# Performance work log

Hardware: AMD Instinct MI355X
Metric: run time of the kernel (lower is better)

The kernel has to match this reference:

```python
import jax, jax.numpy as jnp
import numpy as np
from jax import lax

B, N, M, NCLS = 16, 8192, 64, 80          # batch, anchors, GT boxes, classes
M_W, M_H = 640, 640                       # config.model_in_sz
CLASS_ID = 0                              # config.objective_class_id
PROB_T = 0.0                              # prob_threshold default
IOU_MATCH = 0.5                           # GT<->pred matching threshold
NMS_THR = 0.5                             # NMS IoU threshold
EPS = 1e-7


def xywh2xyxy(x):
    cx, cy, w, h = x[..., 0], x[..., 1], x[..., 2], x[..., 3]
    return jnp.stack([cx - w / 2, cy - h / 2, cx + w / 2, cy + h / 2], axis=-1)


def box_iou(a, b):
    # torchvision-style IoU (no +1), a: (M,4), b: (N,4) -> (M,N)
    area_a = (a[:, 2] - a[:, 0]) * (a[:, 3] - a[:, 1])
    area_b = (b[:, 2] - b[:, 0]) * (b[:, 3] - b[:, 1])
    lt = jnp.maximum(a[:, None, :2], b[None, :, :2])
    rb = jnp.minimum(a[:, None, 2:], b[None, :, 2:])
    wh = jnp.clip(rb - lt, 0)
    inter = wh[..., 0] * wh[..., 1]
    return inter / (area_a[:, None] + area_b[None, :] - inter)


def setup_inputs() -> dict:
    key = jax.random.key(0)
    k1, k2, k3, k4, k5 = jax.random.split(key, 5)
    # GT labels: [class_id, cx, cy, w, h] normalized to [0,1]
    cxy = jax.random.uniform(k1, (B, M, 2), minval=0.2, maxval=0.8)
    wh = jax.random.uniform(k2, (B, M, 2), minval=0.05, maxval=0.25)
    cls = jnp.zeros((B, M, 1), jnp.float32)
    label_batch = jnp.concatenate([cls, cxy, wh], axis=-1)  # (B, M, 5)
    # Predictions: each anchor is a GT box (pixel xywh) + small noise, so
    # IoU>=0.5 matching and NMS actually fire.
    gt_idx = jnp.arange(N) % M
    scale = jnp.array([M_W, M_H, M_W, M_H], jnp.float32)
    base = label_batch[:, gt_idx, 1:] * scale               # (B, N, 4)
    pred_xywh = base + jax.random.normal(k3, (B, N, 4)) * 2.0
    obj = jax.random.uniform(k4, (B, N, 1), minval=0.1, maxval=1.0)
    cls_logits = jax.random.uniform(k5, (B, N, NCLS))
    output = jnp.concatenate([pred_xywh, obj, cls_logits], axis=-1)  # (B,N,85)
    return {"output": output, "label_batch": label_batch}


def nms_keep(boxes, scores, valid):
    # Greedy NMS over a padded candidate set. `valid` marks real candidates;
    # invalid entries get -inf score and can never suppress anything.
    n = boxes.shape[0]
    order = jnp.argsort(jnp.where(valid, scores, -jnp.inf))[::-1]
    b = boxes[order]
    v = valid[order]
    x1, y1, x2, y2 = b[:, 0], b[:, 1], b[:, 2], b[:, 3]
    area = (x2 - x1 + 1) * (y2 - y1 + 1)   # +1 convention, as in the source nms
    pos = jnp.arange(n)

    def body(i, supp):
        active = v[i] & jnp.logical_not(supp[i])
        xx1 = jnp.maximum(x1[i], x1)
        yy1 = jnp.maximum(y1[i], y1)
        xx2 = jnp.minimum(x2[i], x2)
        yy2 = jnp.minimum(y2[i], y2)
        inter = jnp.clip(xx2 - xx1 + 1, 0) * jnp.clip(yy2 - yy1 + 1, 0)
        iou = inter / (area[i] + area - inter + EPS)
        return supp | (active & (pos > i) & (iou > NMS_THR))

    supp = lax.fori_loop(0, n, body, jnp.zeros(n, dtype=bool))
    return v & jnp.logical_not(supp), order


def _per_image(out, lab):
    pred_boxes = xywh2xyxy(out[:, :4])                      # (N,4) pixel xyxy
    obj = out[:, 4]
    logits = out[:, 5 + CLASS_ID] * obj                     # class prob * objectness
    scale = jnp.array([M_W, M_H, M_W, M_H], out.dtype)
    gt = jnp.clip(xywh2xyxy(lab[:, 1:]), 0, 1) * scale      # (M,4) pixel xyxy
    iou = box_iou(gt, pred_boxes)                           # (M,N)
    # candidate = passes prob threshold AND overlaps some GT with IoU>=0.5
    valid = (obj >= PROB_T) & jnp.any(iou >= IOU_MATCH, axis=0)
    keep, order = nms_keep(lax.stop_gradient(pred_boxes),
                           lax.stop_gradient(logits), valid)
    kept = keep.astype(out.dtype)
    return jnp.sum(logits[order] * kept) / jnp.sum(kept)


def reference(output, label_batch):
    loss = jax.vmap(_per_image)(output, label_batch)        # (B,)
    return loss[None, :]                                    # (1, B)
```

## Files before the change

### kernel.cpp

```cpp
#include <hip/hip_runtime.h>
#include <math.h>

#define BB 16
#define NN 8192
#define MM 64
#define ROW 85
#define EPS_F 1e-7f

#define NT1 256
#define NT2 1024
#define NW  16
#define CPW 4
#define CAPB 8

typedef unsigned long long u64;

__global__ void prep_kernel(const float* __restrict__ outp,
                            const float* __restrict__ lab,
                            float4* __restrict__ boxes,
                            float* __restrict__ keys) {
    __shared__ float4 gbox[MM];
    __shared__ float garea[MM];
    const int b = blockIdx.x;
    const int tid = threadIdx.x;
    if (tid < MM) {
        const float* lr = lab + ((size_t)b * MM + tid) * 5;
        float cx = lr[1], cy = lr[2], w = lr[3], h = lr[4];
        float x1 = fminf(fmaxf(cx - w * 0.5f, 0.f), 1.f) * 640.f;
        float y1 = fminf(fmaxf(cy - h * 0.5f, 0.f), 1.f) * 640.f;
        float x2 = fminf(fmaxf(cx + w * 0.5f, 0.f), 1.f) * 640.f;
        float y2 = fminf(fmaxf(cy + h * 0.5f, 0.f), 1.f) * 640.f;
        gbox[tid] = make_float4(x1, y1, x2, y2);
        garea[tid] = (x2 - x1) * (y2 - y1);
    }
    __syncthreads();
    const int n = blockIdx.y * NT1 + tid;
    const float* row = outp + ((size_t)b * NN + n) * ROW;
    float cx = row[0], cy = row[1], w = row[2], h = row[3];
    float obj = row[4], c0 = row[5];
    float px1 = cx - w * 0.5f, py1 = cy - h * 0.5f;
    float px2 = cx + w * 0.5f, py2 = cy + h * 0.5f;
    float pa = (px2 - px1) * (py2 - py1);

    const int m0 = n & (MM - 1);
    bool match;
    {
        float4 g = gbox[m0];
        float iw = fmaxf(fminf(px2, g.z) - fmaxf(px1, g.x), 0.f);
        float ih = fmaxf(fminf(py2, g.w) - fmaxf(py1, g.y), 0.f);
        float inter = iw * ih;
        match = (inter / (garea[m0] + pa - inter) >= 0.5f);
    }
    if (!match) {
        for (int m = 0; m < MM; ++m) {
            float4 g = gbox[m];
            float iw = fmaxf(fminf(px2, g.z) - fmaxf(px1, g.x), 0.f);
            float ih = fmaxf(fminf(py2, g.w) - fmaxf(py1, g.y), 0.f);
            float inter = iw * ih;
            match = match || (inter / (garea[m] + pa - inter) >= 0.5f);
        }
    }
    bool valid = (obj >= 0.0f) && match;
    size_t bn = (size_t)b * NN + ((n & 63) * 128 + (n >> 6));
    boxes[bn] = make_float4(px1, py1, px2, py2);
    keys[bn] = valid ? (c0 * obj) : -INFINITY;
}

__device__ __forceinline__ float wave_fold_max(float x) {
#define DPP_STEPX(ctrl)                                                          \
    { int _o = __builtin_amdgcn_update_dpp(__float_as_int(x), __float_as_int(x), \
                                           (ctrl), 0xF, 0xF, false);             \
      x = fmaxf(x, __int_as_float(_o)); }
    DPP_STEPX(0x111) DPP_STEPX(0x112) DPP_STEPX(0x114)
    DPP_STEPX(0x118) DPP_STEPX(0x142) DPP_STEPX(0x143)
#undef DPP_STEPX
    return x;
}
__device__ __forceinline__ float wave_fold_min(float x) {
#define DPP_STEPN(ctrl)                                                          \
    { int _o = __builtin_amdgcn_update_dpp(__float_as_int(x), __float_as_int(x), \
                                           (ctrl), 0xF, 0xF, false);             \
      x = fminf(x, __int_as_float(_o)); }
    DPP_STEPN(0x111) DPP_STEPN(0x112) DPP_STEPN(0x114)
    DPP_STEPN(0x118) DPP_STEPN(0x142) DPP_STEPN(0x143)
#undef DPP_STEPN
    return x;
}
__device__ __forceinline__ float wave_max64(float x) {
    return __int_as_float(__builtin_amdgcn_readlane(__float_as_int(wave_fold_max(x)), 63));
}
__device__ __forceinline__ float wave_sum64(float x) {
#define DPP_ADD(ctrl)                                                            \
    { int _o = __builtin_amdgcn_update_dpp(0, __float_as_int(x),                 \
                                           (ctrl), 0xF, 0xF, true);              \
      x += __int_as_float(_o); }
    DPP_ADD(0x111) DPP_ADD(0x112) DPP_ADD(0x114)
    DPP_ADD(0x118) DPP_ADD(0x142) DPP_ADD(0x143)
#undef DPP_ADD
    return __int_as_float(__builtin_amdgcn_readlane(__float_as_int(x), 63));
}
__device__ __forceinline__ float bcastlane(float v, int l) {
    return __int_as_float(__builtin_amdgcn_readlane(__float_as_int(v), l));
}

#define KILL_TEST(AK, K_)  do {                                                  \
    float _xx1 = fmaxf(bj.x, x1[K_]), _yy1 = fmaxf(bj.y, y1[K_]);                \
    float _xx2 = fminf(bj.z, x2[K_]), _yy2 = fminf(bj.w, y2[K_]);                \
    float _iw = fmaxf(_xx2 - _xx1 + 1.f, 0.f);                                   \
    float _ih = fmaxf(_yy2 - _yy1 + 1.f, 0.f);                                   \
    float _in = _iw * _ih;                                                       \
    if (sj > ps[K_] && 1.5f * _in > hbj + ha[K_]) (AK) = -INFINITY;              \
} while (0)

__global__ void __launch_bounds__(NT2)
nms_kernel(const float4* __restrict__ boxes, const float* __restrict__ keys,
           float* __restrict__ loss) {
    __shared__ float4 clusterBB[MM];
    __shared__ float  clusterMinA[MM];
    __shared__ u64    adjL[MM];
    __shared__ float4 keptBoxL[MM][CAPB];
    __shared__ float2 keptMetaL[MM][CAPB];
    __shared__ u64    kMask0[MM];
    __shared__ u64    kMask1[MM];
    __shared__ int    keptCnt[MM];
    __shared__ unsigned int chMask[3][2];
    __shared__ float  waveSum[NW];
    __shared__ int    waveCnt[NW];

    const int b = blockIdx.x;
    const int tid = threadIdx.x;
    const int wid = tid >> 6;
    const int lane = tid & 63;
    const size_t base = (size_t)b * NN;

    float x1[8], y1[8], x2[8], y2[8], ha[8], ps[8];
#pragma unroll
    for (int q = 0; q < CPW; ++q) {
#pragma unroll
        for (int s = 0; s < 2; ++s) {
            const int k = q * 2 + s;
            const int c = CPW * wid + q;
            int idx = c * 128 + s * 64 + lane;
            float4 bb = boxes[base + idx];
            x1[k] = bb.x; y1[k] = bb.y; x2[k] = bb.z; y2[k] = bb.w;
            ps[k] = keys[base + idx];
            ha[k] = 0.5f * ((x2[k] - x1[k] + 1.f) * (y2[k] - y1[k] + 1.f));
        }
    }

#pragma unroll
    for (int q = 0; q < CPW; ++q) {
        const int k0 = 2 * q, k1 = 2 * q + 1;
        float mx = INFINITY, my = INFINITY, Mx = -INFINITY, My = -INFINITY, mA = INFINITY;
        if (ps[k0] != -INFINITY) { mx = x1[k0]; my = y1[k0]; Mx = x2[k0]; My = y2[k0]; mA = 2.f * ha[k0]; }
        if (ps[k1] != -INFINITY) { mx = fminf(mx, x1[k1]); my = fminf(my, y1[k1]);
                                   Mx = fmaxf(Mx, x2[k1]); My = fmaxf(My, y2[k1]);
                                   mA = fminf(mA, 2.f * ha[k1]); }
        mx = wave_fold_min(mx); my = wave_fold_min(my);
        Mx = wave_fold_max(Mx); My = wave_fold_max(My);
        mA = wave_fold_min(mA);
        if (lane == 63) {
            clusterBB[CPW * wid + q] = make_float4(mx, my, Mx, My);
            clusterMinA[CPW * wid + q] = mA;
        }
    }
    __syncthreads();

    if (wid == 0) {
        const int t = lane;
        float4 bbT = clusterBB[t];
        float  maT = clusterMinA[t];
        u64 adj = 0ull;
        for (int j = 0; j < MM; ++j) {
            float4 bbJ = clusterBB[j];
            float  maJ = clusterMinA[j];
            float iw = fminf(bbT.z, bbJ.z) - fmaxf(bbT.x, bbJ.x) + 1.f;
            float ih = fminf(bbT.w, bbJ.w) - fmaxf(bbT.y, bbJ.y) + 1.f;
            if (j != t && iw > 0.f && ih > 0.f) {
                float I = iw * ih;
                bool noe = (3.f * I < maT + maJ) || (2.f * I < fmaxf(maT, maJ));
                if (!noe) adj |= (1ull << j);
            }
        }
        adjL[t] = adj;
        kMask0[t] = 0ull; kMask1[t] = 0ull;
        keptCnt[t] = 0;
        if (t == 0) {
            chMask[0][0] = 0xFFFFFFFFu; chMask[0][1] = 0xFFFFFFFFu;
            chMask[1][0] = 0u; chMask[1][1] = 0u;
            chMask[2][0] = 0u; chMask[2][1] = 0u;
        }
    }
    __syncthreads();

    int rr = 0;
    for (; rr < 8200; ++rr) {
        const int cur = rr % 3, nxt = (rr + 1) % 3, clr = (rr + 2) % 3;
        const u64 cm = ((u64)chMask[cur][1] << 32) | (u64)chMask[cur][0];
        if (cm == 0ull) break;
        if (tid == 0) { chMask[clr][0] = 0u; chMask[clr][1] = 0u; }
#pragma unroll
        for (int q = 0; q < CPW; ++q) {
            const int c = CPW * wid + q;
            if (((adjL[c] | (1ull << c)) & cm) == 0ull) continue;

            u64 om0 = kMask0[c], om1 = kMask1[c];
            float a0 = ps[2 * q], a1 = ps[2 * q + 1];
            float4 CBc = clusterBB[c];
            float mha = 0.5f * clusterMinA[c];

            bool flag = false;
            {
                const u64 adjc = adjL[c];
                if ((adjc >> lane) & 1ull) {
                    int K = keptCnt[lane];
                    if (K > CAPB) flag = true;
                    int KB = K < CAPB ? K : CAPB;
                    for (int t2 = 0; t2 < KB; ++t2) {
                        float4 bj = keptBoxL[lane][t2];
                        float2 mt = keptMetaL[lane][t2];
                        float iwS = fminf(bj.z, CBc.z) - fmaxf(bj.x, CBc.x) + 1.f;
                        float ihS = fminf(bj.w, CBc.w) - fmaxf(bj.y, CBc.y) + 1.f;
                        if (iwS > 0.f && ihS > 0.f && 1.5f * (iwS * ihS) > mt.y + mha)
                            flag = true;
                    }
                }
            }
            u64 passM = __ballot(flag);

            while (passM) {
                int ac = __ffsll(passM) - 1; passM &= (passM - 1);
                int K = keptCnt[ac];
                int KB = K < CAPB ? K : CAPB;
                for (int t2 = 0; t2 < KB; ++t2) {
                    float4 bj = keptBoxL[ac][t2];
                    float2 mt = keptMetaL[ac][t2];
                    float iwS = fminf(bj.z, CBc.z) - fmaxf(bj.x, CBc.x) + 1.f;
                    float ihS = fminf(bj.w, CBc.w) - fmaxf(bj.y, CBc.y) + 1.f;
                    if (iwS > 0.f && ihS > 0.f && 1.5f * (iwS * ihS) > mt.y + mha) {
                        float sj = mt.x, hbj = mt.y;
                        KILL_TEST(a0, 2 * q);
                        KILL_TEST(a1, 2 * q + 1);
                    }
                }
                if (K > CAPB) {
                    u64 mm = kMask0[ac];
                    while (mm) {
                        int bit = __ffsll(mm) - 1; mm &= (mm - 1);
                        int gi = ac * 128 + bit;
                        float4 bj = boxes[base + gi];
                        float sj = keys[base + gi];
                        float hbj = 0.5f * ((bj.z - bj.x + 1.f) * (bj.w - bj.y + 1.f))
                                    + 0.5f * EPS_F;
                        KILL_TEST(a0, 2 * q);
                        KILL_TEST(a1, 2 * q + 1);
                    }
                    mm = kMask1[ac];
                    while (mm) {
                        int bit = __ffsll(mm) - 1; mm &= (mm - 1);
                        int gi = ac * 128 + 64 + bit;
                        float4 bj = boxes[base + gi];
                        float sj = keys[base + gi];
                        float hbj = 0.5f * ((bj.z - bj.x + 1.f) * (bj.w - bj.y + 1.f))
                                    + 0.5f * EPS_F;
                        KILL_TEST(a0, 2 * q);
                        KILL_TEST(a1, 2 * q + 1);
                    }
                }
            }

            bool kept0 = false, kept1 = false;
            int cnt = 0;
            while (true) {
                float lv = fmaxf(a0, a1);
                float wm = wave_max64(lv);
                if (wm == -INFINITY) break;
                u64 bm = __ballot(lv == wm);
                int wl = __ffsll(bm) - 1;
                int la = (a0 == lv) ? 0 : 1;
                float cxa = la ? x1[2 * q + 1] : x1[2 * q];
                float cya = la ? y1[2 * q + 1] : y1[2 * q];
                float cxb = la ? x2[2 * q + 1] : x2[2 * q];
                float cyb = la ? y2[2 * q + 1] : y2[2 * q];
                float cha = la ? ha[2 * q + 1] : ha[2 * q];
                float bx1 = bcastlane(cxa, wl), by1 = bcastlane(cya, wl);
                float bx2 = bcastlane(cxb, wl), by2 = bcastlane(cyb, wl);
                float hcb = bcastlane(cha, wl) + 0.5f * EPS_F;
                if (lane == wl) {
                    if (cnt < CAPB) {
                        keptBoxL[c][cnt] = make_float4(cxa, cya, cxb, cyb);
                        keptMetaL[c][cnt] = make_float2(lv, cha + 0.5f * EPS_F);
                    }
                    if (la == 0) { kept0 = true; a0 = -INFINITY; }
                    else         { kept1 = true; a1 = -INFINITY; }
                }
                cnt++;
                if (a0 != -INFINITY) {
                    const int k = 2 * q;
                    float xx1 = fmaxf(bx1, x1[k]), yy1 = fmaxf(by1, y1[k]);
                    float xx2 = fminf(bx2, x2[k]), yy2 = fminf(by2, y2[k]);
                    float iw = fmaxf(xx2 - xx1 + 1.f, 0.f);
                    float ih = fmaxf(yy2 - yy1 + 1.f, 0.f);
                    if (1.5f * (iw * ih) > hcb + ha[k]) a0 = -INFINITY;
                }
                if (a1 != -INFINITY) {
                    const int k = 2 * q + 1;
                    float xx1 = fmaxf(bx1, x1[k]), yy1 = fmaxf(by1, y1[k]);
                    float xx2 = fminf(bx2, x2[k]), yy2 = fminf(by2, y2[k]);
                    float iw = fmaxf(xx2 - xx1 + 1.f, 0.f);
                    float ih = fmaxf(yy2 - yy1 + 1.f, 0.f);
                    if (1.5f * (iw * ih) > hcb + ha[k]) a1 = -INFINITY;
                }
            }
            u64 m0 = __ballot(kept0);
            u64 m1 = __ballot(kept1);
            if (lane == 0) {
                kMask0[c] = m0; kMask1[c] = m1; keptCnt[c] = cnt;
                if (m0 != om0 || m1 != om1)
                    atomicOr(&chMask[nxt][c >> 5], 1u << (c & 31));
            }
        }
        __syncthreads();
    }

    float s = 0.f; int ccount = 0;
#pragma unroll
    for (int q = 0; q < CPW; ++q) {
        const int c = CPW * wid + q;
        u64 m0 = kMask0[c], m1 = kMask1[c];
        if ((m0 >> lane) & 1ull) s += ps[2 * q];
        if ((m1 >> lane) & 1ull) s += ps[2 * q + 1];
        ccount += (int)__popcll(m0) + (int)__popcll(m1);
    }
    s = wave_sum64(s);
    if (lane == 0) { waveSum[wid] = s; waveCnt[wid] = ccount; }
    __syncthreads();
    if (tid == 0) {
        float tot = 0.f; int ct = 0;
#pragma unroll
        for (int w = 0; w < NW; ++w) { tot += waveSum[w]; ct += waveCnt[w]; }
        loss[b] = tot / (float)ct;
    }
}

extern "C" void kernel_launch(void* const* d_in, const int* in_sizes, int n_in,
                              void* d_out, int out_size, void* d_ws, size_t ws_size,
                              hipStream_t stream) {
    const float* outp = (const float*)d_in[0];
    const float* lab  = (const float*)d_in[1];
    float* loss = (float*)d_out;

    float4* boxes = (float4*)d_ws;
    float*  keys  = (float*)((char*)d_ws + (size_t)BB * NN * sizeof(float4));

    dim3 g1(BB, NN / NT1);
    prep_kernel<<<g1, NT1, 0, stream>>>(outp, lab, boxes, keys);
    nms_kernel<<<BB, NT2, 0, stream>>>(boxes, keys, loss);
}
```

Baseline: 54.70 us.

## Process NMS clusters in descending top-score order with per-slot barriers

Each cluster's top score is computed during the bounding-box pass, and clusters are ranked so that slot q*NW+wid holds the q-th group in descending score order. Boxes are then loaded per ranked cluster. The __syncthreads moves inside the per-slot loop, and the active test also looks at changes already flagged for the next round. High-score clusters therefore settle first and their kept sets propagate within the same round, aiming to reduce the number of fixpoint rounds. In exchange each round has four block barriers instead of one, and there is an extra ranking pass.

```diff
diff --git a/kernel.cpp b/kernel.cpp
--- a/kernel.cpp
+++ b/kernel.cpp
@@ -117,6 +117,8 @@
            float* __restrict__ loss) {
     __shared__ float4 clusterBB[MM];
     __shared__ float  clusterMinA[MM];
+    __shared__ float  topScore[MM];
+    __shared__ int    slotCluster[MM];
     __shared__ u64    adjL[MM];
     __shared__ float4 keptBoxL[MM][CAPB];
     __shared__ float2 keptMetaL[MM][CAPB];
@@ -133,35 +135,30 @@
     const int lane = tid & 63;
     const size_t base = (size_t)b * NN;
 
-    float x1[8], y1[8], x2[8], y2[8], ha[8], ps[8];
 #pragma unroll
     for (int q = 0; q < CPW; ++q) {
+        const int c = CPW * wid + q;
+        float mx = INFINITY, my = INFINITY, Mx = -INFINITY, My = -INFINITY;
+        float mA = INFINITY, tS = -INFINITY;
 #pragma unroll
         for (int s = 0; s < 2; ++s) {
-            const int k = q * 2 + s;
-            const int c = CPW * wid + q;
             int idx = c * 128 + s * 64 + lane;
             float4 bb = boxes[base + idx];
-            x1[k] = bb.x; y1[k] = bb.y; x2[k] = bb.z; y2[k] = bb.w;
-            ps[k] = keys[base + idx];
-            ha[k] = 0.5f * ((x2[k] - x1[k] + 1.f) * (y2[k] - y1[k] + 1.f));
-        }
-    }
-
-#pragma unroll
-    for (int q = 0; q < CPW; ++q) {
-        const int k0 = 2 * q, k1 = 2 * q + 1;
-        float mx = INFINITY, my = INFINITY, Mx = -INFINITY, My = -INFINITY, mA = INFINITY;
-        if (ps[k0] != -INFINITY) { mx = x1[k0]; my = y1[k0]; Mx = x2[k0]; My = y2[k0]; mA = 2.f * ha[k0]; }
-        if (ps[k1] != -INFINITY) { mx = fminf(mx, x1[k1]); my = fminf(my, y1[k1]);
-                                   Mx = fmaxf(Mx, x2[k1]); My = fmaxf(My, y2[k1]);
-                                   mA = fminf(mA, 2.f * ha[k1]); }
+            float sc = keys[base + idx];
+            float ar = (bb.z - bb.x + 1.f) * (bb.w - bb.y + 1.f);
+            if (sc != -INFINITY) {
+                mx = fminf(mx, bb.x); my = fminf(my, bb.y);
+                Mx = fmaxf(Mx, bb.z); My = fmaxf(My, bb.w);
+                mA = fminf(mA, ar);   tS = fmaxf(tS, sc);
+            }
+        }
         mx = wave_fold_min(mx); my = wave_fold_min(my);
         Mx = wave_fold_max(Mx); My = wave_fold_max(My);
-        mA = wave_fold_min(mA);
+        mA = wave_fold_min(mA); tS = wave_fold_max(tS);
         if (lane == 63) {
-            clusterBB[CPW * wid + q] = make_float4(mx, my, Mx, My);
-            clusterMinA[CPW * wid + q] = mA;
+            clusterBB[c] = make_float4(mx, my, Mx, My);
+            clusterMinA[c] = mA;
+            topScore[c] = tS;
         }
     }
     __syncthreads();
@@ -185,6 +182,13 @@
         adjL[t] = adj;
         kMask0[t] = 0ull; kMask1[t] = 0ull;
         keptCnt[t] = 0;
+        float myS = topScore[t];
+        int r = 0;
+        for (int j = 0; j < MM; ++j) {
+            float sj = topScore[j];
+            r += (sj > myS || (sj == myS && j < t)) ? 1 : 0;
+        }
+        slotCluster[r] = t;
         if (t == 0) {
             chMask[0][0] = 0xFFFFFFFFu; chMask[0][1] = 0xFFFFFFFFu;
             chMask[1][0] = 0u; chMask[1][1] = 0u;
@@ -193,140 +197,160 @@
     }
     __syncthreads();
 
-    int rr = 0;
-    for (; rr < 8200; ++rr) {
+    int cq[CPW];
+#pragma unroll
+    for (int q = 0; q < CPW; ++q) cq[q] = slotCluster[q * NW + wid];
+
+    float x1[8], y1[8], x2[8], y2[8], ha[8], ps[8];
+#pragma unroll
+    for (int q = 0; q < CPW; ++q) {
+#pragma unroll
+        for (int s = 0; s < 2; ++s) {
+            const int k = q * 2 + s;
+            int idx = cq[q] * 128 + s * 64 + lane;
+            float4 bb = boxes[base + idx];
+            x1[k] = bb.x; y1[k] = bb.y; x2[k] = bb.z; y2[k] = bb.w;
+            ps[k] = keys[base + idx];
+            ha[k] = 0.5f * ((x2[k] - x1[k] + 1.f) * (y2[k] - y1[k] + 1.f));
+        }
+    }
+
+    for (int rr = 0; rr < 8200; ++rr) {
         const int cur = rr % 3, nxt = (rr + 1) % 3, clr = (rr + 2) % 3;
         const u64 cm = ((u64)chMask[cur][1] << 32) | (u64)chMask[cur][0];
         if (cm == 0ull) break;
         if (tid == 0) { chMask[clr][0] = 0u; chMask[clr][1] = 0u; }
 #pragma unroll
         for (int q = 0; q < CPW; ++q) {
-            const int c = CPW * wid + q;
-            if (((adjL[c] | (1ull << c)) & cm) == 0ull) continue;
-
-            u64 om0 = kMask0[c], om1 = kMask1[c];
-            float a0 = ps[2 * q], a1 = ps[2 * q + 1];
-            float4 CBc = clusterBB[c];
-            float mha = 0.5f * clusterMinA[c];
-
-            bool flag = false;
-            {
-                const u64 adjc = adjL[c];
-                if ((adjc >> lane) & 1ull) {
-                    int K = keptCnt[lane];
-                    if (K > CAPB) flag = true;
+            const int c = cq[q];
+            const u64 fresh = cm |
+                (((u64)chMask[nxt][1] << 32) | (u64)chMask[nxt][0]);
+            bool active = ((adjL[c] | (1ull << c)) & fresh) != 0ull;
+            if (active) {
+                u64 om0 = kMask0[c], om1 = kMask1[c];
+                float a0 = ps[2 * q], a1 = ps[2 * q + 1];
+                float4 CBc = clusterBB[c];
+                float mha = 0.5f * clusterMinA[c];
+
+                bool flag = false;
+                {
+                    const u64 adjc = adjL[c];
+                    if ((adjc >> lane) & 1ull) {
+                        int K = keptCnt[lane];
+                        if (K > CAPB) flag = true;
+                        int KB = K < CAPB ? K : CAPB;
+                        for (int t2 = 0; t2 < KB; ++t2) {
+                            float4 bj = keptBoxL[lane][t2];
+                            float2 mt = keptMetaL[lane][t2];
+                            float iwS = fminf(bj.z, CBc.z) - fmaxf(bj.x, CBc.x) + 1.f;
+                            float ihS = fminf(bj.w, CBc.w) - fmaxf(bj.y, CBc.y) + 1.f;
+                            if (iwS > 0.f && ihS > 0.f && 1.5f * (iwS * ihS) > mt.y + mha)
+                                flag = true;
+                        }
+                    }
+                }
+                u64 passM = __ballot(flag);
+
+                while (passM) {
+                    int ac = __ffsll(passM) - 1; passM &= (passM - 1);
+                    int K = keptCnt[ac];
                     int KB = K < CAPB ? K : CAPB;
                     for (int t2 = 0; t2 < KB; ++t2) {
-                        float4 bj = keptBoxL[lane][t2];
-                        float2 mt = keptMetaL[lane][t2];
+                        float4 bj = keptBoxL[ac][t2];
+                        float2 mt = keptMetaL[ac][t2];
                         float iwS = fminf(bj.z, CBc.z) - fmaxf(bj.x, CBc.x) + 1.f;
                         float ihS = fminf(bj.w, CBc.w) - fmaxf(bj.y, CBc.y) + 1.f;
-                        if (iwS > 0.f && ihS > 0.f && 1.5f * (iwS * ihS) > mt.y + mha)
-                            flag = true;
-                    }
+                        if (iwS > 0.f && ihS > 0.f && 1.5f * (iwS * ihS) > mt.y + mha) {
+                            float sj = mt.x, hbj = mt.y;
+                            KILL_TEST(a0, 2 * q);
+                            KILL_TEST(a1, 2 * q + 1);
+                        }
+                    }
+                    if (K > CAPB) {
+                        u64 mm = kMask0[ac];
+                        while (mm) {
+                            int bit = __ffsll(mm) - 1; mm &= (mm - 1);
+                            int gi = ac * 128 + bit;
+                            float4 bj = boxes[base + gi];
+                            float sj = keys[base + gi];
+                            float hbj = 0.5f * ((bj.z - bj.x + 1.f) * (bj.w - bj.y + 1.f))
+                                        + 0.5f * EPS_F;
+                            KILL_TEST(a0, 2 * q);
+                            KILL_TEST(a1, 2 * q + 1);
+                        }
+                        mm = kMask1[ac];
+                        while (mm) {
+                            int bit = __ffsll(mm) - 1; mm &= (mm - 1);
+                            int gi = ac * 128 + 64 + bit;
+                            float4 bj = boxes[base + gi];
+                            float sj = keys[base + gi];
+                            float hbj = 0.5f * ((bj.z - bj.x + 1.f) * (bj.w - bj.y + 1.f))
+                                        + 0.5f * EPS_F;
+                            KILL_TEST(a0, 2 * q);
+                            KILL_TEST(a1, 2 * q + 1);
+                        }
+                    }
+                }
+
+                bool kept0 = false, kept1 = false;
+                int cnt = 0;
+                while (true) {
+                    float lv = fmaxf(a0, a1);
+                    float wm = wave_max64(lv);
+                    if (wm == -INFINITY) break;
+                    u64 bm = __ballot(lv == wm);
+                    int wl = __ffsll(bm) - 1;
+                    int la = (a0 == lv) ? 0 : 1;
+                    float cxa = la ? x1[2 * q + 1] : x1[2 * q];
+                    float cya = la ? y1[2 * q + 1] : y1[2 * q];
+                    float cxb = la ? x2[2 * q + 1] : x2[2 * q];
+                    float cyb = la ? y2[2 * q + 1] : y2[2 * q];
+                    float cha = la ? ha[2 * q + 1] : ha[2 * q];
+                    float bx1 = bcastlane(cxa, wl), by1 = bcastlane(cya, wl);
+                    float bx2 = bcastlane(cxb, wl), by2 = bcastlane(cyb, wl);
+                    float hcb = bcastlane(cha, wl) + 0.5f * EPS_F;
+                    if (lane == wl) {
+                        if (cnt < CAPB) {
+                            keptBoxL[c][cnt] = make_float4(cxa, cya, cxb, cyb);
+                            keptMetaL[c][cnt] = make_float2(lv, cha + 0.5f * EPS_F);
+                        }
+                        if (la == 0) { kept0 = true; a0 = -INFINITY; }
+                        else         { kept1 = true; a1 = -INFINITY; }
+                    }
+                    cnt++;
+                    if (a0 != -INFINITY) {
+                        const int k = 2 * q;
+                        float xx1 = fmaxf(bx1, x1[k]), yy1 = fmaxf(by1, y1[k]);
+                        float xx2 = fminf(bx2, x2[k]), yy2 = fminf(by2, y2[k]);
+                        float iw = fmaxf(xx2 - xx1 + 1.f, 0.f);
+                        float ih = fmaxf(yy2 - yy1 + 1.f, 0.f);
+                        if (1.5f * (iw * ih) > hcb + ha[k]) a0 = -INFINITY;
+                    }
+                    if (a1 != -INFINITY) {
+                        const int k = 2 * q + 1;
+                        float xx1 = fmaxf(bx1, x1[k]), yy1 = fmaxf(by1, y1[k]);
+                        float xx2 = fminf(bx2, x2[k]), yy2 = fminf(by2, y2[k]);
+                        float iw = fmaxf(xx2 - xx1 + 1.f, 0.f);
+                        float ih = fmaxf(yy2 - yy1 + 1.f, 0.f);
+                        if (1.5f * (iw * ih) > hcb + ha[k]) a1 = -INFINITY;
+                    }
+                }
+                u64 m0 = __ballot(kept0);
+                u64 m1 = __ballot(kept1);
+                if (lane == 0) {
+                    kMask0[c] = m0; kMask1[c] = m1; keptCnt[c] = cnt;
+                    if (m0 != om0 || m1 != om1)
+                        atomicOr(&chMask[nxt][c >> 5], 1u << (c & 31));
                 }
             }
-            u64 passM = __ballot(flag);
-
-            while (passM) {
-                int ac = __ffsll(passM) - 1; passM &= (passM - 1);
-                int K = keptCnt[ac];
-                int KB = K < CAPB ? K : CAPB;
-                for (int t2 = 0; t2 < KB; ++t2) {
-                    float4 bj = keptBoxL[ac][t2];
-                    float2 mt = keptMetaL[ac][t2];
-                    float iwS = fminf(bj.z, CBc.z) - fmaxf(bj.x, CBc.x) + 1.f;
-                    float ihS = fminf(bj.w, CBc.w) - fmaxf(bj.y, CBc.y) + 1.f;
-                    if (iwS > 0.f && ihS > 0.f && 1.5f * (iwS * ihS) > mt.y + mha) {
-                        float sj = mt.x, hbj = mt.y;
-                        KILL_TEST(a0, 2 * q);
-                        KILL_TEST(a1, 2 * q + 1);
-                    }
-                }
-                if (K > CAPB) {
-                    u64 mm = kMask0[ac];
-                    while (mm) {
-                        int bit = __ffsll(mm) - 1; mm &= (mm - 1);
-                        int gi = ac * 128 + bit;
-                        float4 bj = boxes[base + gi];
-                        float sj = keys[base + gi];
-                        float hbj = 0.5f * ((bj.z - bj.x + 1.f) * (bj.w - bj.y + 1.f))
-                                    + 0.5f * EPS_F;
-                        KILL_TEST(a0, 2 * q);
-                        KILL_TEST(a1, 2 * q + 1);
-                    }
-                    mm = kMask1[ac];
-                    while (mm) {
-                        int bit = __ffsll(mm) - 1; mm &= (mm - 1);
-                        int gi = ac * 128 + 64 + bit;
-                        float4 bj = boxes[base + gi];
-                        float sj = keys[base + gi];
-                        float hbj = 0.5f * ((bj.z - bj.x + 1.f) * (bj.w - bj.y + 1.f))
-                                    + 0.5f * EPS_F;
-                        KILL_TEST(a0, 2 * q);
-                        KILL_TEST(a1, 2 * q + 1);
-                    }
-                }
-            }
-
-            bool kept0 = false, kept1 = false;
-            int cnt = 0;
-            while (true) {
-                float lv = fmaxf(a0, a1);
-                float wm = wave_max64(lv);
-                if (wm == -INFINITY) break;
-                u64 bm = __ballot(lv == wm);
-                int wl = __ffsll(bm) - 1;
-                int la = (a0 == lv) ? 0 : 1;
-                float cxa = la ? x1[2 * q + 1] : x1[2 * q];
-                float cya = la ? y1[2 * q + 1] : y1[2 * q];
-                float cxb = la ? x2[2 * q + 1] : x2[2 * q];
-                float cyb = la ? y2[2 * q + 1] : y2[2 * q];
-                float cha = la ? ha[2 * q + 1] : ha[2 * q];
-                float bx1 = bcastlane(cxa, wl), by1 = bcastlane(cya, wl);
-                float bx2 = bcastlane(cxb, wl), by2 = bcastlane(cyb, wl);
-                float hcb = bcastlane(cha, wl) + 0.5f * EPS_F;
-                if (lane == wl) {
-                    if (cnt < CAPB) {
-                        keptBoxL[c][cnt] = make_float4(cxa, cya, cxb, cyb);
-                        keptMetaL[c][cnt] = make_float2(lv, cha + 0.5f * EPS_F);
-                    }
-                    if (la == 0) { kept0 = true; a0 = -INFINITY; }
-                    else         { kept1 = true; a1 = -INFINITY; }
-                }
-                cnt++;
-                if (a0 != -INFINITY) {
-                    const int k = 2 * q;
-                    float xx1 = fmaxf(bx1, x1[k]), yy1 = fmaxf(by1, y1[k]);
-                    float xx2 = fminf(bx2, x2[k]), yy2 = fminf(by2, y2[k]);
-                    float iw = fmaxf(xx2 - xx1 + 1.f, 0.f);
-                    float ih = fmaxf(yy2 - yy1 + 1.f, 0.f);
-                    if (1.5f * (iw * ih) > hcb + ha[k]) a0 = -INFINITY;
-                }
-                if (a1 != -INFINITY) {
-                    const int k = 2 * q + 1;
-                    float xx1 = fmaxf(bx1, x1[k]), yy1 = fmaxf(by1, y1[k]);
-                    float xx2 = fminf(bx2, x2[k]), yy2 = fminf(by2, y2[k]);
-                    float iw = fmaxf(xx2 - xx1 + 1.f, 0.f);
-                    float ih = fmaxf(yy2 - yy1 + 1.f, 0.f);
-                    if (1.5f * (iw * ih) > hcb + ha[k]) a1 = -INFINITY;
-                }
-            }
-            u64 m0 = __ballot(kept0);
-            u64 m1 = __ballot(kept1);
-            if (lane == 0) {
-                kMask0[c] = m0; kMask1[c] = m1; keptCnt[c] = cnt;
-                if (m0 != om0 || m1 != om1)
-                    atomicOr(&chMask[nxt][c >> 5], 1u << (c & 31));
-            }
-        }
-        __syncthreads();
+            __syncthreads();
+        }
     }
 
     float s = 0.f; int ccount = 0;
 #pragma unroll
     for (int q = 0; q < CPW; ++q) {
-        const int c = CPW * wid + q;
+        const int c = cq[q];
         u64 m0 = kMask0[c], m1 = kMask1[c];
         if ((m0 >> lane) & 1ull) s += ps[2 * q];
         if ((m1 >> lane) & 1ull) s += ps[2 * q + 1];
```

Result: slower. 87.57 us (+60.1%).
